# Kernel tuning notes

Hardware: AMD Instinct MI355X
Metric: run time of the kernel (lower is better)

The kernel has to match this reference:

```python
import jax, jax.numpy as jnp
import numpy as np

NUM_ANCHORS = 5
NUM_CLASSES = 20


def setup_inputs() -> dict:
    key = jax.random.key(0)
    k1, k2, k3, k4 = jax.random.split(key, 4)
    N, H, W, M = 64, 52, 52, 32
    img = 1664
    x = jax.random.normal(k1, (N, NUM_ANCHORS * (5 + NUM_CLASSES), H, W), jnp.float32)
    anchors = jnp.array([[1.08, 1.19], [3.42, 4.41], [6.63, 11.38],
                         [9.42, 5.11], [16.62, 10.52]], jnp.float32)
    # valid gt boxes in xyxy pixel coords
    xy = jax.random.uniform(k2, (N, M, 2), jnp.float32) * (img * 0.8)
    wh = jax.random.uniform(k3, (N, M, 2), jnp.float32) * (img * 0.2) + 1.0
    gt_boxes = jnp.concatenate([xy, xy + wh], axis=-1)
    gt_labels = jax.random.randint(k4, (N, M), 0, NUM_CLASSES)
    return dict(x=x, anchors=anchors, gt_boxes=gt_boxes, gt_labels=gt_labels,
                img_h=img, img_w=img)


def _format_outputs(x, anchors, img_h, img_w):
    # x: [N, A*(5+C), H, W] -> (coords [N,HW,A,4] (x,y,w,h), obj [N,HW,A], scores [N,HW,A,C])
    N, _, H, W = x.shape
    A = anchors.shape[0]
    t = x.reshape(N, A, 5 + NUM_CLASSES, H, W).transpose(0, 3, 4, 1, 2)  # [N,H,W,A,5+C]
    c_x = jnp.arange(W, dtype=x.dtype) * (img_w / W)
    c_y = jnp.arange(H, dtype=x.dtype) * (img_h / H)
    b_x = jax.nn.sigmoid(t[..., 0]) + c_x[None, None, :, None]   # [N,H,W,A]
    b_y = jax.nn.sigmoid(t[..., 1]) + c_y[None, :, None, None]
    b_w = (img_w / W) * anchors[:, 0] * jnp.exp(t[..., 2])
    b_h = (img_h / H) * anchors[:, 1] * jnp.exp(t[..., 3])
    coords = jnp.stack([b_x, b_y, b_w, b_h], axis=-1).reshape(N, H * W, A, 4)
    b_o = jax.nn.sigmoid(t[..., 4]).reshape(N, H * W, A)
    scores = t[..., 5:].reshape(N, H * W, A, NUM_CLASSES)
    return coords, b_o, scores


def reference(x, anchors, gt_boxes, gt_labels, img_h, img_w):
    coords, b_o, scores = _format_outputs(x, anchors, img_h, img_w)
    # pred_boxes[..., 2:] += pred_boxes[..., :2]  (xywh -> xyxy)
    boxes = jnp.concatenate([coords[..., :2], coords[..., :2] + coords[..., 2:]], axis=-1)  # [N,HW,A,4]
    # box_iou: pred [N,HW,A,1,4] vs gt [N,1,1,M,4] -> [N,HW,A,M]
    p = boxes[..., None, :]
    g = gt_boxes[:, None, None, :, :]
    lt = jnp.maximum(p[..., :2], g[..., :2])
    rb = jnp.minimum(p[..., 2:], g[..., 2:])
    whi = jnp.clip(rb - lt, 0.0)
    inter = whi[..., 0] * whi[..., 1]
    area_p = (boxes[..., 2] - boxes[..., 0]) * (boxes[..., 3] - boxes[..., 1])
    area_g = (gt_boxes[..., 2] - gt_boxes[..., 0]) * (gt_boxes[..., 3] - gt_boxes[..., 1])
    iou = inter / (area_p[..., None] + area_g[:, None, None, :] - inter)   # [N,HW,A,M]

    cell_sel = iou.max(axis=(2, 3)) > 0.0                 # [N,HW]
    best_a = jnp.argmax(iou.max(axis=3), axis=2)          # [N,HW] best anchor per cell
    iou_best = jnp.take_along_axis(iou, best_a[..., None, None], axis=2)[:, :, 0, :]  # [N,HW,M]
    max_iou = iou_best.max(axis=-1)                       # [N,HW]
    gt_idx = jnp.argmax(iou_best, axis=-1)                # [N,HW]

    sel_box = jnp.take_along_axis(boxes, best_a[..., None, None], axis=2)[:, :, 0, :]   # [N,HW,4]
    sel_o = jnp.take_along_axis(b_o, best_a[..., None], axis=2)[:, :, 0]                # [N,HW]
    sel_sc = jnp.take_along_axis(scores, best_a[..., None, None], axis=2)[:, :, 0, :]   # [N,HW,C]
    g_box = jnp.take_along_axis(gt_boxes, gt_idx[..., None], axis=1)                    # [N,HW,4]
    g_lab = jnp.take_along_axis(gt_labels, gt_idx, axis=1)                              # [N,HW]

    m = cell_sel.astype(x.dtype)
    objectness_loss = (jnp.sum(m * (sel_o - max_iou) ** 2)
                       + 0.5 * jnp.sum((1.0 - m) * b_o.max(axis=2) ** 2))
    bbox_loss = (jnp.sum(m * jnp.sum((sel_box[..., :2] - g_box[..., :2]) ** 2, axis=-1))
                 + jnp.sum(m * jnp.sum((jnp.sqrt(sel_box[..., 2:]) - jnp.sqrt(g_box[..., 2:])) ** 2, axis=-1)))
    logp = jax.nn.log_softmax(sel_sc, axis=-1)
    ce = -jnp.take_along_axis(logp, g_lab[..., None], axis=-1)[..., 0]
    clf_loss = jnp.sum(m * ce)
    return jnp.stack([objectness_loss, bbox_loss, clf_loss])
```

## Files before the change

kernel.cpp:

```cpp
#include <hip/hip_runtime.h>
#include <math.h>

#define A_ 5
#define C_ 20
#define N_ 64
#define H_ 52
#define W_ 52
#define HW_ (H_ * W_)
#define M_ 32
#define CH_ (A_ * (5 + C_))
#define CPB 256
#define NBLK_X ((HW_ + CPB - 1) / CPB)
#define NBLK (NBLK_X * N_)

__global__ __launch_bounds__(320, 3) void yolo_main(
    const float* __restrict__ x,
    const float* __restrict__ anchors,
    const float* __restrict__ gt,
    const int* __restrict__ glab,
    const void* img_h_p, const void* img_w_p,
    float* __restrict__ ws)
{
    __shared__ float s_c[5][A_][CPB];

    const int tid  = threadIdx.x;
    const int a    = tid >> 6;
    const int lane = tid & 63;
    const int n    = blockIdx.y;
    const int cb   = blockIdx.x * CPB + lane * 4;
    const bool valid = cb < HW_;

    int ibw = *(const int*)img_w_p;
    float img_w = (ibw > 0 && ibw < 1000000) ? (float)ibw : *(const float*)img_w_p;
    int ibh = *(const int*)img_h_p;
    float img_h = (ibh > 0 && ibh < 1000000) ? (float)ibh : *(const float*)img_h_p;
    const float sx = img_w / (float)W_;
    const float sy = img_h / (float)H_;

    const float ax = anchors[2 * a];
    const float ay = anchors[2 * a + 1];

    float bi[4] = {0.f, 0.f, 0.f, 0.f};
    float bu[4] = {1.f, 1.f, 1.f, 1.f};
    int   bm[4] = {0, 0, 0, 0};
    float ov[4] = {0.f, 0.f, 0.f, 0.f};
    float ce[4] = {0.f, 0.f, 0.f, 0.f};
    float bb[4] = {0.f, 0.f, 0.f, 0.f};

    if (valid) {
        const size_t base = (size_t)n * CH_ * HW_ + (size_t)a * 25 * HW_ + cb;

        float4 S[C_];
        #pragma unroll
        for (int j = 0; j < C_; ++j)
            S[j] = *(const float4*)(x + base + (size_t)(5 + j) * HW_);
        float4 T0 = *(const float4*)(x + base);
        float4 T1 = *(const float4*)(x + base + (size_t)HW_);
        float4 T2 = *(const float4*)(x + base + 2 * (size_t)HW_);
        float4 T3 = *(const float4*)(x + base + 3 * (size_t)HW_);
        float4 T4 = *(const float4*)(x + base + 4 * (size_t)HW_);

        float lse[4];
        {
            const float* Sf = (const float*)S;
            #pragma unroll
            for (int k = 0; k < 4; ++k) {
                float mx = Sf[k];
                #pragma unroll
                for (int j = 1; j < C_; ++j) mx = fmaxf(mx, Sf[j * 4 + k]);
                float se = 0.f;
                #pragma unroll
                for (int j = 0; j < C_; ++j) se += __expf(Sf[j * 4 + k] - mx);
                lse[k] = mx + __logf(se);
            }
        }

        float x1[4], y1[4], x2[4], y2[4], ap[4];
        {
            const float* t0 = (const float*)&T0;
            const float* t1 = (const float*)&T1;
            const float* t2 = (const float*)&T2;
            const float* t3 = (const float*)&T3;
            const float* t4 = (const float*)&T4;
            #pragma unroll
            for (int k = 0; k < 4; ++k) {
                const int c  = cb + k;
                const int wi = c % W_;
                const int hi = c / W_;
                float bx = 1.f / (1.f + __expf(-t0[k])) + (float)wi * sx;
                float by = 1.f / (1.f + __expf(-t1[k])) + (float)hi * sy;
                float bw = sx * ax * __expf(t2[k]);
                float bh = sy * ay * __expf(t3[k]);
                x1[k] = bx; y1[k] = by; x2[k] = bx + bw; y2[k] = by + bh;
                ov[k] = 1.f / (1.f + __expf(-t4[k]));
                ap[k] = (x2[k] - x1[k]) * (y2[k] - y1[k]);
            }
        }

        const float4* gtv = (const float4*)(gt + (size_t)n * M_ * 4);
        #pragma unroll 4
        for (int m = 0; m < M_; ++m) {
            float4 g = gtv[m];
            float area = (g.z - g.x) * (g.w - g.y);
            #pragma unroll
            for (int k = 0; k < 4; ++k) {
                float wxi = fminf(x2[k], g.z) - fmaxf(x1[k], g.x);
                float hyi = fminf(y2[k], g.w) - fmaxf(y1[k], g.y);
                wxi = fmaxf(wxi, 0.f);
                hyi = fmaxf(hyi, 0.f);
                float inter = wxi * hyi;
                float uni = ap[k] + area - inter;
                if (inter * bu[k] > bi[k] * uni) { bi[k] = inter; bu[k] = uni; bm[k] = m; }
            }
        }

        #pragma unroll
        for (int k = 0; k < 4; ++k) {
            float4 g = ((const float4*)gt)[n * M_ + bm[k]];
            int lab = glab[n * M_ + bm[k]];
            float d0 = x1[k] - g.x;
            float d1 = y1[k] - g.y;
            float d2 = sqrtf(x2[k]) - sqrtf(g.z);
            float d3 = sqrtf(y2[k]) - sqrtf(g.w);
            bb[k] = d0 * d0 + d1 * d1 + d2 * d2 + d3 * d3;
            float sval = x[base + (size_t)(5 + lab) * HW_ + k];
            ce[k] = lse[k] - sval;
        }
    }

    if (valid) {
        const int cl = lane * 4;
        #pragma unroll
        for (int k = 0; k < 4; ++k) {
            s_c[0][a][cl + k] = bi[k];
            s_c[1][a][cl + k] = bu[k];
            s_c[2][a][cl + k] = ov[k];
            s_c[3][a][cl + k] = ce[k];
            s_c[4][a][cl + k] = bb[k];
        }
    }
    __syncthreads();

    float obj = 0.f, bbx = 0.f, clf = 0.f;
    if (tid < 256 && (blockIdx.x * CPB + tid) < HW_) {
        const int t = tid;
        float Bi = 0.f, Bu = 1.f, O = 0.f, CE = 0.f, BB = 0.f;
        float bomax = -1e30f;
        #pragma unroll
        for (int aa = 0; aa < A_; ++aa) {
            float ci = s_c[0][aa][t];
            float cu = s_c[1][aa][t];
            float co = s_c[2][aa][t];
            bomax = fmaxf(bomax, co);
            bool upd = (aa == 0) || (ci * Bu > Bi * cu);
            if (upd) {
                Bi = ci; Bu = cu; O = co;
                CE = s_c[3][aa][t];
                BB = s_c[4][aa][t];
            }
        }
        if (Bi > 0.f) {
            float d = O - Bi / Bu;
            obj = d * d;
            bbx = BB;
            clf = CE;
        } else {
            obj = 0.5f * bomax * bomax;
        }
    }

    #pragma unroll
    for (int off = 32; off > 0; off >>= 1) {
        obj += __shfl_down(obj, off, 64);
        bbx += __shfl_down(bbx, off, 64);
        clf += __shfl_down(clf, off, 64);
    }
    __shared__ float s_red[5][3];
    if ((tid & 63) == 0) {
        const int wid = tid >> 6;
        s_red[wid][0] = obj; s_red[wid][1] = bbx; s_red[wid][2] = clf;
    }
    __syncthreads();
    if (tid == 0) {
        float oo = 0.f, bs = 0.f, cc = 0.f;
        #pragma unroll
        for (int w = 0; w < 5; ++w) {
            oo += s_red[w][0]; bs += s_red[w][1]; cc += s_red[w][2];
        }
        const int bid = blockIdx.y * gridDim.x + blockIdx.x;
        ws[0 * NBLK + bid] = oo;
        ws[1 * NBLK + bid] = bs;
        ws[2 * NBLK + bid] = cc;
    }
}

__global__ __launch_bounds__(1024) void yolo_reduce(
    const float* __restrict__ ws, float* __restrict__ out)
{
    __shared__ float s_red[16][3];
    const int tid = threadIdx.x;
    float o = 0.f, b = 0.f, c = 0.f;
    for (int e = tid; e < NBLK; e += 1024) {
        o += ws[0 * NBLK + e];
        b += ws[1 * NBLK + e];
        c += ws[2 * NBLK + e];
    }
    #pragma unroll
    for (int off = 32; off > 0; off >>= 1) {
        o += __shfl_down(o, off, 64);
        b += __shfl_down(b, off, 64);
        c += __shfl_down(c, off, 64);
    }
    const int wid = tid >> 6;
    if ((tid & 63) == 0) {
        s_red[wid][0] = o; s_red[wid][1] = b; s_red[wid][2] = c;
    }
    __syncthreads();
    if (tid == 0) {
        float oo = 0.f, bb = 0.f, cc = 0.f;
        #pragma unroll
        for (int w = 0; w < 16; ++w) {
            oo += s_red[w][0]; bb += s_red[w][1]; cc += s_red[w][2];
        }
        out[0] = oo; out[1] = bb; out[2] = cc;
    }
}

extern "C" void kernel_launch(void* const* d_in, const int* in_sizes, int n_in,
                              void* d_out, int out_size, void* d_ws, size_t ws_size,
                              hipStream_t stream) {
    (void)in_sizes; (void)n_in; (void)out_size; (void)ws_size;
    const float* x    = (const float*)d_in[0];
    const float* anch = (const float*)d_in[1];
    const float* gt   = (const float*)d_in[2];
    const int*   gl   = (const int*)d_in[3];
    const void*  ih   = d_in[4];
    const void*  iw   = d_in[5];
    float* out = (float*)d_out;
    float* ws  = (float*)d_ws;

    dim3 grid(NBLK_X, N_);
    yolo_main<<<grid, dim3(320), 0, stream>>>(x, anch, gt, gl, ih, iw, ws);
    yolo_reduce<<<1, 1024, 0, stream>>>(ws, out);
}
```

Before: 159.0 us.

## Halve cells per thread and split IoU argmax into two independent chains

Each thread now handles 2 cells instead of 4, using float2 loads. Blocks cover 128 cells, and the grid doubles to about 1408 blocks. Launch bounds rise to 5 blocks per CU, aiming to cut register pressure, raise occupancy and hide memory latency. The IoU argmax loop now keeps two independent best-candidate chains over even and odd gt boxes and merges them at the end, which adds instruction-level parallelism but can change tie-breaking order. With 128 cells per block, the final per-cell stage uses only two of the five waves, and the reduction has twice as many partials.

```diff
diff --git a/kernel.cpp b/kernel.cpp
--- a/kernel.cpp
+++ b/kernel.cpp
@@ -9,11 +9,11 @@
 #define HW_ (H_ * W_)
 #define M_ 32
 #define CH_ (A_ * (5 + C_))
-#define CPB 256
-#define NBLK_X ((HW_ + CPB - 1) / CPB)
-#define NBLK (NBLK_X * N_)
-
-__global__ __launch_bounds__(320, 3) void yolo_main(
+#define CPB 128
+#define NBX ((HW_ + CPB - 1) / CPB)
+#define NBLK (NBX * N_)
+
+__global__ __launch_bounds__(320, 5) void yolo_main(
     const float* __restrict__ x,
     const float* __restrict__ anchors,
     const float* __restrict__ gt,
@@ -27,7 +27,7 @@
     const int a    = tid >> 6;
     const int lane = tid & 63;
     const int n    = blockIdx.y;
-    const int cb   = blockIdx.x * CPB + lane * 4;
+    const int cb   = blockIdx.x * CPB + lane * 2;
     const bool valid = cb < HW_;
 
     int ibw = *(const int*)img_w_p;
@@ -40,42 +40,42 @@
     const float ax = anchors[2 * a];
     const float ay = anchors[2 * a + 1];
 
-    float bi[4] = {0.f, 0.f, 0.f, 0.f};
-    float bu[4] = {1.f, 1.f, 1.f, 1.f};
-    int   bm[4] = {0, 0, 0, 0};
-    float ov[4] = {0.f, 0.f, 0.f, 0.f};
-    float ce[4] = {0.f, 0.f, 0.f, 0.f};
-    float bb[4] = {0.f, 0.f, 0.f, 0.f};
+    float bi[2] = {0.f, 0.f};
+    float bu[2] = {1.f, 1.f};
+    int   bm[2] = {0, 0};
+    float ov[2] = {0.f, 0.f};
+    float ce[2] = {0.f, 0.f};
+    float bb[2] = {0.f, 0.f};
 
     if (valid) {
         const size_t base = (size_t)n * CH_ * HW_ + (size_t)a * 25 * HW_ + cb;
 
-        float4 S[C_];
+        float2 T0 = *(const float2*)(x + base);
+        float2 T1 = *(const float2*)(x + base + (size_t)HW_);
+        float2 T2 = *(const float2*)(x + base + 2 * (size_t)HW_);
+        float2 T3 = *(const float2*)(x + base + 3 * (size_t)HW_);
+        float2 T4 = *(const float2*)(x + base + 4 * (size_t)HW_);
+        float2 S[C_];
         #pragma unroll
         for (int j = 0; j < C_; ++j)
-            S[j] = *(const float4*)(x + base + (size_t)(5 + j) * HW_);
-        float4 T0 = *(const float4*)(x + base);
-        float4 T1 = *(const float4*)(x + base + (size_t)HW_);
-        float4 T2 = *(const float4*)(x + base + 2 * (size_t)HW_);
-        float4 T3 = *(const float4*)(x + base + 3 * (size_t)HW_);
-        float4 T4 = *(const float4*)(x + base + 4 * (size_t)HW_);
-
-        float lse[4];
+            S[j] = *(const float2*)(x + base + (size_t)(5 + j) * HW_);
+
+        float lse[2];
         {
             const float* Sf = (const float*)S;
             #pragma unroll
-            for (int k = 0; k < 4; ++k) {
+            for (int k = 0; k < 2; ++k) {
                 float mx = Sf[k];
                 #pragma unroll
-                for (int j = 1; j < C_; ++j) mx = fmaxf(mx, Sf[j * 4 + k]);
+                for (int j = 1; j < C_; ++j) mx = fmaxf(mx, Sf[j * 2 + k]);
                 float se = 0.f;
                 #pragma unroll
-                for (int j = 0; j < C_; ++j) se += __expf(Sf[j * 4 + k] - mx);
+                for (int j = 0; j < C_; ++j) se += __expf(Sf[j * 2 + k] - mx);
                 lse[k] = mx + __logf(se);
             }
         }
 
-        float x1[4], y1[4], x2[4], y2[4], ap[4];
+        float x1[2], y1[2], x2[2], y2[2], ap[2];
         {
             const float* t0 = (const float*)&T0;
             const float* t1 = (const float*)&T1;
@@ -83,7 +83,7 @@
             const float* t3 = (const float*)&T3;
             const float* t4 = (const float*)&T4;
             #pragma unroll
-            for (int k = 0; k < 4; ++k) {
+            for (int k = 0; k < 2; ++k) {
                 const int c  = cb + k;
                 const int wi = c % W_;
                 const int hi = c / W_;
@@ -97,25 +97,50 @@
             }
         }
 
+        float cbi[2][2] = {{0.f, 0.f}, {0.f, 0.f}};
+        float cbu[2][2] = {{1.f, 1.f}, {1.f, 1.f}};
+        int   cbm[2][2] = {{0, 1}, {0, 1}};
         const float4* gtv = (const float4*)(gt + (size_t)n * M_ * 4);
         #pragma unroll 4
-        for (int m = 0; m < M_; ++m) {
-            float4 g = gtv[m];
-            float area = (g.z - g.x) * (g.w - g.y);
+        for (int m = 0; m < M_; m += 2) {
+            float4 g0 = gtv[m];
+            float4 g1 = gtv[m + 1];
+            float ar0 = (g0.z - g0.x) * (g0.w - g0.y);
+            float ar1 = (g1.z - g1.x) * (g1.w - g1.y);
             #pragma unroll
-            for (int k = 0; k < 4; ++k) {
-                float wxi = fminf(x2[k], g.z) - fmaxf(x1[k], g.x);
-                float hyi = fminf(y2[k], g.w) - fmaxf(y1[k], g.y);
-                wxi = fmaxf(wxi, 0.f);
-                hyi = fmaxf(hyi, 0.f);
-                float inter = wxi * hyi;
-                float uni = ap[k] + area - inter;
-                if (inter * bu[k] > bi[k] * uni) { bi[k] = inter; bu[k] = uni; bm[k] = m; }
-            }
-        }
-
-        #pragma unroll
-        for (int k = 0; k < 4; ++k) {
+            for (int k = 0; k < 2; ++k) {
+                {
+                    float wq = fminf(x2[k], g0.z) - fmaxf(x1[k], g0.x);
+                    float hq = fminf(y2[k], g0.w) - fmaxf(y1[k], g0.y);
+                    wq = fmaxf(wq, 0.f); hq = fmaxf(hq, 0.f);
+                    float inter = wq * hq;
+                    float uni = ap[k] + ar0 - inter;
+                    if (inter * cbu[k][0] > cbi[k][0] * uni) {
+                        cbi[k][0] = inter; cbu[k][0] = uni; cbm[k][0] = m;
+                    }
+                }
+                {
+                    float wq = fminf(x2[k], g1.z) - fmaxf(x1[k], g1.x);
+                    float hq = fminf(y2[k], g1.w) - fmaxf(y1[k], g1.y);
+                    wq = fmaxf(wq, 0.f); hq = fmaxf(hq, 0.f);
+                    float inter = wq * hq;
+                    float uni = ap[k] + ar1 - inter;
+                    if (inter * cbu[k][1] > cbi[k][1] * uni) {
+                        cbi[k][1] = inter; cbu[k][1] = uni; cbm[k][1] = m + 1;
+                    }
+                }
+            }
+        }
+        #pragma unroll
+        for (int k = 0; k < 2; ++k) {
+            bool c1 = cbi[k][1] * cbu[k][0] > cbi[k][0] * cbu[k][1];
+            bi[k] = c1 ? cbi[k][1] : cbi[k][0];
+            bu[k] = c1 ? cbu[k][1] : cbu[k][0];
+            bm[k] = c1 ? cbm[k][1] : cbm[k][0];
+        }
+
+        #pragma unroll
+        for (int k = 0; k < 2; ++k) {
             float4 g = ((const float4*)gt)[n * M_ + bm[k]];
             int lab = glab[n * M_ + bm[k]];
             float d0 = x1[k] - g.x;
@@ -129,9 +154,9 @@
     }
 
     if (valid) {
-        const int cl = lane * 4;
-        #pragma unroll
-        for (int k = 0; k < 4; ++k) {
+        const int cl = lane * 2;
+        #pragma unroll
+        for (int k = 0; k < 2; ++k) {
             s_c[0][a][cl + k] = bi[k];
             s_c[1][a][cl + k] = bu[k];
             s_c[2][a][cl + k] = ov[k];
@@ -142,7 +167,7 @@
     __syncthreads();
 
     float obj = 0.f, bbx = 0.f, clf = 0.f;
-    if (tid < 256 && (blockIdx.x * CPB + tid) < HW_) {
+    if (tid < CPB && (blockIdx.x * CPB + tid) < HW_) {
         const int t = tid;
         float Bi = 0.f, Bu = 1.f, O = 0.f, CE = 0.f, BB = 0.f;
         float bomax = -1e30f;
@@ -239,7 +264,7 @@
     float* out = (float*)d_out;
     float* ws  = (float*)d_ws;
 
-    dim3 grid(NBLK_X, N_);
+    dim3 grid(NBX, N_);
     yolo_main<<<grid, dim3(320), 0, stream>>>(x, anch, gt, gl, ih, iw, ws);
     yolo_reduce<<<1, 1024, 0, stream>>>(ws, out);
 }
```

Result: faster. 146.9 us (-7.6%).
